# Performance work log

Hardware: AMD Instinct MI355X
Metric: run time of the kernel (lower is better)

The kernel has to match this reference:

```python
import jax, jax.numpy as jnp
import numpy as np

N_NODES = 100000
NODES_PER_GRAPH = 100
IN_CHANNELS = 256
RATIO = 0.5


def setup_inputs() -> dict:
    key = jax.random.key(0)
    k_x, k_w, k_b = jax.random.split(key, 3)
    x = jax.random.normal(k_x, (N_NODES, IN_CHANNELS), dtype=jnp.float32)
    # sorted per-node graph ids: 1000 graphs of 100 nodes each
    batch = (jnp.arange(N_NODES, dtype=jnp.int64) // NODES_PER_GRAPH).astype(jnp.int64)
    # Linear(in_channels, 1): weight [1, d], bias [1] (torch default init scale)
    bound = 1.0 / np.sqrt(IN_CHANNELS)
    W = jax.random.uniform(k_w, (1, IN_CHANNELS), dtype=jnp.float32, minval=-bound, maxval=bound)
    b = jax.random.uniform(k_b, (1,), dtype=jnp.float32, minval=-bound, maxval=bound)
    return {"x": x, "batch": batch, "W": W, "b": b}


def reference(x, batch, W, b):
    N = x.shape[0]
    num_graphs = int(batch[-1]) + 1          # static under equal-size segments
    n_per = N // num_graphs
    k = int(np.ceil(RATIO * n_per))          # PyG topk: ceil(ratio * n_i)

    # linear score: [N]
    scores = x @ W[0] + b[0]

    # per-graph segment top-k (segments are equal-size, contiguous)
    grid = scores.reshape(num_graphs, n_per)                  # [G, n_per]
    top_vals, top_idx = jax.lax.top_k(grid, k)                # each [G, k], descending

    offsets = (jnp.arange(num_graphs, dtype=top_idx.dtype) * n_per)[:, None]
    node_index = (top_idx + offsets).reshape(-1)              # [G*k] global node ids
    weight = top_vals.reshape(-1)                             # scores[node_index]
    cluster_index = jnp.arange(node_index.shape[0], dtype=node_index.dtype)
    return node_index, cluster_index, weight
```

## Files before the change

kernel.cpp:

```cpp
#include <hip/hip_runtime.h>
#include <hip/hip_bf16.h>


#define NPG   100
#define DIM   256
#define KSEL  50
#define ROWS_PER_WAVE 16
#define ROWS_PER_BLOCK 64

typedef float vfloat4 __attribute__((ext_vector_type(4)));

static __device__ __forceinline__ float bf2f(unsigned short s) {
    union { unsigned int u; float f; } v;
    v.u = ((unsigned int)s) << 16;
    return v.f;
}

static __device__ __forceinline__ bool probe_f32(const void* xv) {
    const unsigned short* xu = (const unsigned short*)xv;
    bool f32 = false;
    #pragma unroll
    for (int i = 0; i < 64; ++i) {
        const float v = bf2f(xu[2 * i]);
        if (!(v > -64.0f && v < 64.0f)) f32 = true;
    }
    return f32;
}

__global__ __launch_bounds__(256, 4) void gemv_scores_kernel(
    const void* __restrict__ xv,
    const void* __restrict__ Wv,
    const void* __restrict__ bv,
    float* __restrict__ scores,
    int n_rows)
{
    __shared__ float w_sh[DIM];

    const int tid  = threadIdx.x;
    const int wave = tid >> 6;
    const int lane = tid & 63;

    const bool f32 = probe_f32(xv);

    if (f32) w_sh[tid] = ((const float*)Wv)[tid];
    else     w_sh[tid] = bf2f(((const unsigned short*)Wv)[tid]);
    __syncthreads();

    const float bval = f32 ? ((const float*)bv)[0]
                           : bf2f(((const unsigned short*)bv)[0]);
    const float wl0 = w_sh[lane * 4 + 0];
    const float wl1 = w_sh[lane * 4 + 1];
    const float wl2 = w_sh[lane * 4 + 2];
    const float wl3 = w_sh[lane * 4 + 3];

    const int row0 = blockIdx.x * ROWS_PER_BLOCK + wave * ROWS_PER_WAVE;

    if (f32) {
        const vfloat4* xr = (const vfloat4*)xv;
        vfloat4 u[ROWS_PER_WAVE];
        #pragma unroll
        for (int i = 0; i < ROWS_PER_WAVE; ++i) {
            const int r = row0 + i;
            if (r < n_rows)
                u[i] = __builtin_nontemporal_load(&xr[(size_t)r * (DIM / 4) + lane]);
            else
                u[i] = (vfloat4){0.f, 0.f, 0.f, 0.f};
        }
        #pragma unroll
        for (int i = 0; i < ROWS_PER_WAVE; ++i) {
            const int r = row0 + i;
            float acc = u[i].x * wl0 + u[i].y * wl1 + u[i].z * wl2 + u[i].w * wl3;
            #pragma unroll
            for (int off = 32; off > 0; off >>= 1)
                acc += __shfl_down(acc, off, 64);
            if (lane == 0 && r < n_rows) scores[r] = acc + bval;
        }
    } else {
        const unsigned short* x = (const unsigned short*)xv;
        for (int i = 0; i < ROWS_PER_WAVE; ++i) {
            const int r = row0 + i;
            if (r >= n_rows) break;
            const ushort4 u = ((const ushort4*)(x + (size_t)r * DIM))[lane];
            float acc = bf2f(u.x) * wl0 + bf2f(u.y) * wl1
                      + bf2f(u.z) * wl2 + bf2f(u.w) * wl3;
            #pragma unroll
            for (int off = 32; off > 0; off >>= 1)
                acc += __shfl_down(acc, off, 64);
            if (lane == 0) scores[r] = acc + bval;
        }
    }
}

__global__ __launch_bounds__(128) void select_kernel(
    const void* __restrict__ xv,
    const float* __restrict__ scores,
    void* __restrict__ outv,
    int num_graphs)
{
    __shared__ float sc[NPG];

    const int g   = blockIdx.x;
    const int tid = threadIdx.x;

    const bool f32 = probe_f32(xv);

    if (tid < NPG) sc[tid] = scores[g * NPG + tid];
    __syncthreads();

    if (tid < NPG) {
        const float v = sc[tid];
        int rank = 0;
        #pragma unroll 4
        for (int i = 0; i < NPG; ++i) {
            const float vi = sc[i];
            rank += (vi > v) || (vi == v && i < tid);
        }
        if (rank < KSEL) {
            const int total = num_graphs * KSEL;
            const int pos   = g * KSEL + rank;
            const int node  = g * NPG + tid;
            if (f32) {
                float* o = (float*)outv;
                o[pos]             = (float)node;
                o[total + pos]     = (float)pos;
                o[2 * total + pos] = v;
            } else {
                __hip_bfloat16* o = (__hip_bfloat16*)outv;
                o[pos]             = __float2bfloat16((float)node);
                o[total + pos]     = __float2bfloat16((float)pos);
                o[2 * total + pos] = __float2bfloat16(v);
            }
        }
    }
}

extern "C" void kernel_launch(void* const* d_in, const int* in_sizes, int n_in,
                              void* d_out, int out_size, void* d_ws, size_t ws_size,
                              hipStream_t stream) {
    int xi = -1, wi = -1, bi = -1;
    long best = -1;
    for (int i = 0; i < n_in; ++i) {
        const long s = in_sizes[i];
        if (s > best) { best = s; xi = i; }
    }
    for (int i = 0; i < n_in; ++i) {
        if (i == xi) continue;
        const long s = in_sizes[i];
        if (s == DIM && wi < 0) wi = i;
        if (s == 1   && bi < 0) bi = i;
    }
    if (xi < 0) xi = 0;
    if (wi < 0) wi = (n_in > 2) ? 2 : 1;
    if (bi < 0) bi = n_in - 1;

    const long n_rows     = (long)in_sizes[xi] / DIM;
    const long num_graphs = n_rows / NPG;
    if (num_graphs <= 0) return;

    float* scores_ws = (float*)d_ws;

    const unsigned grid_a = (unsigned)((n_rows + ROWS_PER_BLOCK - 1) / ROWS_PER_BLOCK);
    gemv_scores_kernel<<<dim3(grid_a), dim3(256), 0, stream>>>(
        d_in[xi], d_in[wi], d_in[bi], scores_ws, (int)n_rows);

    select_kernel<<<dim3((unsigned)num_graphs), dim3(128), 0, stream>>>(
        d_in[xi], scores_ws, d_out, (int)num_graphs);
}
```

Before: 156.9 us.

## Fuse score GEMV and per-graph top-k selection into one kernel

Merges the GEMV score kernel and the per-graph rank-selection kernel into one kernel with one block per graph. Each of the four waves computes 25 rows' scores straight into shared memory, so the global scores buffer round trip and the second launch go away. The bf16 path now batches its loads like the f32 path. In exchange the grid shrinks to 1000 blocks of 256 threads with 25 outstanding 16-byte loads per lane, and the launch-bounds occupancy hint is dropped.

```diff
diff --git a/kernel.cpp b/kernel.cpp
--- a/kernel.cpp
+++ b/kernel.cpp
@@ -5,8 +5,7 @@
 #define NPG   100
 #define DIM   256
 #define KSEL  50
-#define ROWS_PER_WAVE 16
-#define ROWS_PER_BLOCK 64
+#define ROWS_PER_WAVE 25
 
 typedef float vfloat4 __attribute__((ext_vector_type(4)));
 
@@ -27,18 +26,20 @@
     return f32;
 }
 
-__global__ __launch_bounds__(256, 4) void gemv_scores_kernel(
+__global__ __launch_bounds__(256) void fused_select_kernel(
     const void* __restrict__ xv,
     const void* __restrict__ Wv,
     const void* __restrict__ bv,
-    float* __restrict__ scores,
-    int n_rows)
+    void* __restrict__ outv,
+    int num_graphs)
 {
     __shared__ float w_sh[DIM];
+    __shared__ float sc[NPG];
 
     const int tid  = threadIdx.x;
     const int wave = tid >> 6;
     const int lane = tid & 63;
+    const int g    = blockIdx.x;
 
     const bool f32 = probe_f32(xv);
 
@@ -53,58 +54,40 @@
     const float wl2 = w_sh[lane * 4 + 2];
     const float wl3 = w_sh[lane * 4 + 3];
 
-    const int row0 = blockIdx.x * ROWS_PER_BLOCK + wave * ROWS_PER_WAVE;
+    const int rbase = wave * ROWS_PER_WAVE;
+    const long grow0 = (long)g * NPG + rbase;
 
     if (f32) {
         const vfloat4* xr = (const vfloat4*)xv;
         vfloat4 u[ROWS_PER_WAVE];
         #pragma unroll
-        for (int i = 0; i < ROWS_PER_WAVE; ++i) {
-            const int r = row0 + i;
-            if (r < n_rows)
-                u[i] = __builtin_nontemporal_load(&xr[(size_t)r * (DIM / 4) + lane]);
-            else
-                u[i] = (vfloat4){0.f, 0.f, 0.f, 0.f};
-        }
+        for (int i = 0; i < ROWS_PER_WAVE; ++i)
+            u[i] = __builtin_nontemporal_load(
+                       &xr[(size_t)(grow0 + i) * (DIM / 4) + lane]);
         #pragma unroll
         for (int i = 0; i < ROWS_PER_WAVE; ++i) {
-            const int r = row0 + i;
             float acc = u[i].x * wl0 + u[i].y * wl1 + u[i].z * wl2 + u[i].w * wl3;
             #pragma unroll
             for (int off = 32; off > 0; off >>= 1)
                 acc += __shfl_down(acc, off, 64);
-            if (lane == 0 && r < n_rows) scores[r] = acc + bval;
+            if (lane == 0) sc[rbase + i] = acc + bval;
         }
     } else {
         const unsigned short* x = (const unsigned short*)xv;
+        ushort4 u[ROWS_PER_WAVE];
+        #pragma unroll
+        for (int i = 0; i < ROWS_PER_WAVE; ++i)
+            u[i] = ((const ushort4*)(x + (size_t)(grow0 + i) * DIM))[lane];
+        #pragma unroll
         for (int i = 0; i < ROWS_PER_WAVE; ++i) {
-            const int r = row0 + i;
-            if (r >= n_rows) break;
-            const ushort4 u = ((const ushort4*)(x + (size_t)r * DIM))[lane];
-            float acc = bf2f(u.x) * wl0 + bf2f(u.y) * wl1
-                      + bf2f(u.z) * wl2 + bf2f(u.w) * wl3;
+            float acc = bf2f(u[i].x) * wl0 + bf2f(u[i].y) * wl1
+                      + bf2f(u[i].z) * wl2 + bf2f(u[i].w) * wl3;
             #pragma unroll
             for (int off = 32; off > 0; off >>= 1)
                 acc += __shfl_down(acc, off, 64);
-            if (lane == 0) scores[r] = acc + bval;
+            if (lane == 0) sc[rbase + i] = acc + bval;
         }
     }
-}
-
-__global__ __launch_bounds__(128) void select_kernel(
-    const void* __restrict__ xv,
-    const float* __restrict__ scores,
-    void* __restrict__ outv,
-    int num_graphs)
-{
-    __shared__ float sc[NPG];
-
-    const int g   = blockIdx.x;
-    const int tid = threadIdx.x;
-
-    const bool f32 = probe_f32(xv);
-
-    if (tid < NPG) sc[tid] = scores[g * NPG + tid];
     __syncthreads();
 
     if (tid < NPG) {
@@ -157,12 +140,8 @@
     const long num_graphs = n_rows / NPG;
     if (num_graphs <= 0) return;
 
-    float* scores_ws = (float*)d_ws;
+    (void)d_ws; (void)ws_size;
 
-    const unsigned grid_a = (unsigned)((n_rows + ROWS_PER_BLOCK - 1) / ROWS_PER_BLOCK);
-    gemv_scores_kernel<<<dim3(grid_a), dim3(256), 0, stream>>>(
-        d_in[xi], d_in[wi], d_in[bi], scores_ws, (int)n_rows);
-
-    select_kernel<<<dim3((unsigned)num_graphs), dim3(128), 0, stream>>>(
-        d_in[xi], scores_ws, d_out, (int)num_graphs);
+    fused_select_kernel<<<dim3((unsigned)num_graphs), dim3(256), 0, stream>>>(
+        d_in[xi], d_in[wi], d_in[bi], d_out, (int)num_graphs);
 }
```

Measured after the change: 151.0 us. -3.8%, faster.
